# Performance work log

Measured on AMD Instinct MI355X. Metric: run time of the kernel, lower is better.

Reference implementation:

```python
import jax, jax.numpy as jnp
import numpy as np

B, N, M = 16, 4096, 77
Q_DIM, C_DIM = 1024, 768
H, D = 8, 64
INNER = H * D

def setup_inputs() -> dict:
    key = jax.random.key(0)
    ks = jax.random.split(key, 7)
    x = jax.random.normal(ks[0], (B, N, Q_DIM), dtype=jnp.float32)
    context = jax.random.normal(ks[1], (B, M, C_DIM), dtype=jnp.float32)
    # nn.Linear weights (stored as (in, out) for right-multiply), no bias for q/k/v
    Wq = jax.random.normal(ks[2], (Q_DIM, INNER), dtype=jnp.float32) / np.sqrt(Q_DIM)
    Wk = jax.random.normal(ks[3], (C_DIM, INNER), dtype=jnp.float32) / np.sqrt(C_DIM)
    Wv = jax.random.normal(ks[4], (C_DIM, INNER), dtype=jnp.float32) / np.sqrt(C_DIM)
    Wo = jax.random.normal(ks[5], (INNER, Q_DIM), dtype=jnp.float32) / np.sqrt(INNER)
    bo = jax.random.normal(ks[6], (Q_DIM,), dtype=jnp.float32) * 0.01
    return {"x": x, "context": context, "Wq": Wq, "Wk": Wk, "Wv": Wv, "Wo": Wo, "bo": bo}

def reference(x, context, Wq, Wk, Wv, Wo, bo):
    scale = D ** (-0.5)
    q = (x @ Wq).reshape(B, N, H, D).transpose(0, 2, 1, 3)        # (B,H,N,D)
    k = (context @ Wk).reshape(B, M, H, D).transpose(0, 2, 1, 3)  # (B,H,M,D)
    v = (context @ Wv).reshape(B, M, H, D).transpose(0, 2, 1, 3)  # (B,H,M,D)
    attn = jnp.einsum('bhnd,bhmd->bhnm', q, k) * scale            # (B,H,N,M)
    attn = jax.nn.softmax(attn, axis=-1)
    out = jnp.einsum('bhnm,bhmd->bhnd', attn, v)                  # (B,H,N,D)
    out = out.transpose(0, 2, 1, 3).reshape(B, N, INNER)
    return out @ Wo + bo
```

## Files before the change

kernel.cpp:

```cpp
#include <hip/hip_runtime.h>
#include <hip/hip_bf16.h>
#include <stdint.h>


typedef unsigned short u16;
typedef __bf16 bf16x8 __attribute__((ext_vector_type(8)));
typedef float f32x4 __attribute__((ext_vector_type(4)));

__device__ __forceinline__ void gld_lds16(const void* g, void* l) {
  __builtin_amdgcn_global_load_lds(
      (const __attribute__((address_space(1))) unsigned int*)g,
      (__attribute__((address_space(3))) unsigned int*)l, 16, 0, 0);
}

__device__ __forceinline__ u16 f2bf(float f) {
  __hip_bfloat16 h = __float2bfloat16(f);
  return *reinterpret_cast<u16*>(&h);
}

__global__ void wtrans(const float* __restrict__ in, u16* __restrict__ out,
                       int K, int N) {
  int idx = blockIdx.x * 256 + threadIdx.x;
  if (idx < K * N) {
    int n = idx / K, k = idx - n * K;
    out[idx] = f2bf(in[k * N + n]);
  }
}

__global__ void vtrans(const u16* __restrict__ kv_all, u16* __restrict__ vt_all) {
  int idx = blockIdx.x * 256 + threadIdx.x;
  if (idx < 16 * 8 * 64 * 96) {
    int m = idx % 96;
    int t = idx / 96;
    int d = t & 63;
    int bh = t >> 6;
    int b = bh >> 3, h = bh & 7;
    int mg = m < 77 ? m : 76;
    vt_all[idx] = kv_all[(size_t)(b * 77 + mg) * 1024 + 512 + h * 64 + d];
  }
}

template <bool A_F32, bool C_F32>
__global__ __launch_bounds__(256, 2) void gemm_bt(
    const void* __restrict__ Av, const u16* __restrict__ BT,
    void* __restrict__ Cv, const float* __restrict__ bias,
    int Mr, int K, int Nc) {
  __shared__ u16 Al[128 * 32 * (A_F32 ? 2 : 1)];
  __shared__ u16 Bl[128 * 32];
  const int tid = threadIdx.x;
  const int lane = tid & 63;
  const int wave = tid >> 6;
  const int mlane = lane & 15;
  const int quad = lane >> 4;
  const int m0 = blockIdx.y * 128;
  const int n0 = blockIdx.x * 128;
  const int wm = (wave & 1) * 64;
  const int wn = (wave >> 1) * 64;

  f32x4 acc[4][4];
#pragma unroll
  for (int i = 0; i < 4; ++i)
#pragma unroll
    for (int j = 0; j < 4; ++j) acc[i][j] = (f32x4){0.f, 0.f, 0.f, 0.f};

  const int o0 = tid * 16;

  for (int k0 = 0; k0 < K; k0 += 32) {
    if (A_F32) {
#pragma unroll
      for (int r = 0; r < 4; ++r) {
        const int o = r * 4096 + o0;
        const int row = o >> 7;
        const int colb = o & 127;
        int rg = m0 + row;
        rg = rg < Mr ? rg : (Mr - 1);
        gld_lds16((const char*)Av + ((size_t)rg * K + k0) * 4 + colb,
                  (char*)Al + o);
      }
    } else {
#pragma unroll
      for (int r = 0; r < 2; ++r) {
        const int o = r * 4096 + o0;
        const int row = o >> 6;
        const int colb = o & 63;
        int rg = m0 + row;
        rg = rg < Mr ? rg : (Mr - 1);
        gld_lds16((const char*)Av + ((size_t)rg * K + k0) * 2 + colb,
                  (char*)Al + o);
      }
    }
#pragma unroll
    for (int r = 0; r < 2; ++r) {
      const int o = r * 4096 + o0;
      const int row = o >> 6;
      const int colb = o & 63;
      gld_lds16((const char*)BT + ((size_t)(n0 + row) * K + k0) * 2 + colb,
                (char*)Bl + o);
    }
    __syncthreads();

    bf16x8 af[4], bfr[4];
    if (A_F32) {
      const float* Af = (const float*)Al;
#pragma unroll
      for (int i = 0; i < 4; ++i) {
        const float* ar = Af + (wm + i * 16 + mlane) * 32 + quad * 8;
        f32x4 x0 = *(const f32x4*)ar;
        f32x4 x1 = *(const f32x4*)(ar + 4);
        bf16x8 t;
#pragma unroll
        for (int e = 0; e < 4; ++e) {
          u16 lo = f2bf(x0[e]);
          u16 hi = f2bf(x1[e]);
          t[e] = *reinterpret_cast<__bf16*>(&lo);
          t[e + 4] = *reinterpret_cast<__bf16*>(&hi);
        }
        af[i] = t;
      }
    } else {
      const u16* Ab = (const u16*)Al;
#pragma unroll
      for (int i = 0; i < 4; ++i)
        af[i] = *(const bf16x8*)(Ab + (wm + i * 16 + mlane) * 32 + quad * 8);
    }
#pragma unroll
    for (int j = 0; j < 4; ++j)
      bfr[j] = *(const bf16x8*)(Bl + (wn + j * 16 + mlane) * 32 + quad * 8);
#pragma unroll
    for (int i = 0; i < 4; ++i)
#pragma unroll
      for (int j = 0; j < 4; ++j)
        acc[i][j] = __builtin_amdgcn_mfma_f32_16x16x32_bf16(af[i], bfr[j],
                                                            acc[i][j], 0, 0, 0);
    __syncthreads();
  }

#pragma unroll
  for (int j = 0; j < 4; ++j) {
    const int col = n0 + wn + j * 16 + mlane;
    const float bv = C_F32 ? bias[col] : 0.f;
#pragma unroll
    for (int i = 0; i < 4; ++i) {
      const int rb = m0 + wm + i * 16 + quad * 4;
#pragma unroll
      for (int r = 0; r < 4; ++r) {
        const int row = rb + r;
        if (row < Mr) {
          if (C_F32)
            ((float*)Cv)[(size_t)row * Nc + col] = acc[i][j][r] + bv;
          else
            ((u16*)Cv)[(size_t)row * Nc + col] = f2bf(acc[i][j][r]);
        }
      }
    }
  }
}

template <bool A_F32, bool C_F32>
__global__ __launch_bounds__(256, 2) void gemm_bt2(
    const void* __restrict__ Av, const u16* __restrict__ BT,
    void* __restrict__ Cv, const float* __restrict__ bias,
    int Mr, int K, int Nc) {
  __shared__ u16 Al[128 * 32 * (A_F32 ? 2 : 1)];
  __shared__ u16 Bl[256 * 32];
  const int tid = threadIdx.x;
  const int lane = tid & 63;
  const int wave = tid >> 6;
  const int mlane = lane & 15;
  const int quad = lane >> 4;
  const int m0 = blockIdx.y * 128;
  const int n0 = blockIdx.x * 256;
  const int wm = (wave & 1) * 64;
  const int wn = (wave >> 1) * 128;

  f32x4 acc[4][8];
#pragma unroll
  for (int i = 0; i < 4; ++i)
#pragma unroll
    for (int j = 0; j < 8; ++j) acc[i][j] = (f32x4){0.f, 0.f, 0.f, 0.f};

  const int o0 = tid * 16;

  for (int k0 = 0; k0 < K; k0 += 32) {
    if (A_F32) {
#pragma unroll
      for (int r = 0; r < 4; ++r) {
        const int o = r * 4096 + o0;
        const int row = o >> 7;
        const int colb = o & 127;
        int rg = m0 + row;
        rg = rg < Mr ? rg : (Mr - 1);
        gld_lds16((const char*)Av + ((size_t)rg * K + k0) * 4 + colb,
                  (char*)Al + o);
      }
    } else {
#pragma unroll
      for (int r = 0; r < 2; ++r) {
        const int o = r * 4096 + o0;
        const int row = o >> 6;
        const int colb = o & 63;
        int rg = m0 + row;
        rg = rg < Mr ? rg : (Mr - 1);
        gld_lds16((const char*)Av + ((size_t)rg * K + k0) * 2 + colb,
                  (char*)Al + o);
      }
    }
#pragma unroll
    for (int r = 0; r < 4; ++r) {
      const int o = r * 4096 + o0;
      const int row = o >> 6;
      const int colb = o & 63;
      gld_lds16((const char*)BT + ((size_t)(n0 + row) * K + k0) * 2 + colb,
                (char*)Bl + o);
    }
    __syncthreads();

    bf16x8 af[4], bfr[8];
    if (A_F32) {
      const float* Af = (const float*)Al;
#pragma unroll
      for (int i = 0; i < 4; ++i) {
        const float* ar = Af + (wm + i * 16 + mlane) * 32 + quad * 8;
        f32x4 x0 = *(const f32x4*)ar;
        f32x4 x1 = *(const f32x4*)(ar + 4);
        bf16x8 t;
#pragma unroll
        for (int e = 0; e < 4; ++e) {
          u16 lo = f2bf(x0[e]);
          u16 hi = f2bf(x1[e]);
          t[e] = *reinterpret_cast<__bf16*>(&lo);
          t[e + 4] = *reinterpret_cast<__bf16*>(&hi);
        }
        af[i] = t;
      }
    } else {
      const u16* Ab = (const u16*)Al;
#pragma unroll
      for (int i = 0; i < 4; ++i)
        af[i] = *(const bf16x8*)(Ab + (wm + i * 16 + mlane) * 32 + quad * 8);
    }
#pragma unroll
    for (int j = 0; j < 8; ++j)
      bfr[j] = *(const bf16x8*)(Bl + (wn + j * 16 + mlane) * 32 + quad * 8);
#pragma unroll
    for (int i = 0; i < 4; ++i)
#pragma unroll
      for (int j = 0; j < 8; ++j)
        acc[i][j] = __builtin_amdgcn_mfma_f32_16x16x32_bf16(af[i], bfr[j],
                                                            acc[i][j], 0, 0, 0);
    __syncthreads();
  }

#pragma unroll
  for (int j = 0; j < 8; ++j) {
    const int col = n0 + wn + j * 16 + mlane;
    const float bv = C_F32 ? bias[col] : 0.f;
#pragma unroll
    for (int i = 0; i < 4; ++i) {
      const int rb = m0 + wm + i * 16 + quad * 4;
#pragma unroll
      for (int r = 0; r < 4; ++r) {
        const int row = rb + r;
        if (row < Mr) {
          if (C_F32)
            ((float*)Cv)[(size_t)row * Nc + col] = acc[i][j][r] + bv;
          else
            ((u16*)Cv)[(size_t)row * Nc + col] = f2bf(acc[i][j][r]);
        }
      }
    }
  }
}

__global__ __launch_bounds__(256, 2) void attn_mfma(
    const u16* __restrict__ q_all,
    const u16* __restrict__ kv_all,
    const u16* __restrict__ vt_all,
    u16* __restrict__ o_all) {
  __shared__ u16 Ps[128 * 128];
  const int tid = threadIdx.x;
  const int lane = tid & 63;
  const int wave = tid >> 6;
  const int mlane = lane & 15;
  const int quad = lane >> 4;
  const int b = blockIdx.x >> 3;
  const int h = blockIdx.x & 7;
  const int n0 = blockIdx.y * 128;
  const int wm = wave * 32;

  const u16* qbase =
      q_all + ((size_t)(b * 4096 + n0 + wm)) * 512 + h * 64;
  bf16x8 aq[2][2];
#pragma unroll
  for (int i = 0; i < 2; ++i)
#pragma unroll
    for (int ks = 0; ks < 2; ++ks)
      aq[i][ks] = *(const bf16x8*)(qbase + (size_t)(i * 16 + mlane) * 512 +
                                   ks * 32 + quad * 8);

  bf16x8 bk[5][2];
#pragma unroll
  for (int j = 0; j < 5; ++j) {
    int m = j * 16 + mlane;
    m = m < 77 ? m : 76;
    const u16* kb = kv_all + ((size_t)(b * 77 + m)) * 1024 + h * 64;
#pragma unroll
    for (int ks = 0; ks < 2; ++ks)
      bk[j][ks] = *(const bf16x8*)(kb + ks * 32 + quad * 8);
  }

  f32x4 S[2][5];
#pragma unroll
  for (int i = 0; i < 2; ++i)
#pragma unroll
    for (int j = 0; j < 5; ++j) S[i][j] = (f32x4){0.f, 0.f, 0.f, 0.f};
#pragma unroll
  for (int i = 0; i < 2; ++i)
#pragma unroll
    for (int j = 0; j < 5; ++j)
#pragma unroll
      for (int ks = 0; ks < 2; ++ks)
        S[i][j] = __builtin_amdgcn_mfma_f32_16x16x32_bf16(aq[i][ks], bk[j][ks],
                                                          S[i][j], 0, 0, 0);

  float rs[2][4] = {{0.f, 0.f, 0.f, 0.f}, {0.f, 0.f, 0.f, 0.f}};
#pragma unroll
  for (int i = 0; i < 2; ++i)
#pragma unroll
    for (int j = 0; j < 5; ++j) {
      const int col = j * 16 + mlane;
      const bool valid = col < 77;
#pragma unroll
      for (int r = 0; r < 4; ++r) {
        float e = valid ? __expf(S[i][j][r] * 0.125f) : 0.f;
        S[i][j][r] = e;
        rs[i][r] += e;
      }
    }
#pragma unroll
  for (int i = 0; i < 2; ++i)
#pragma unroll
    for (int r = 0; r < 4; ++r) {
      float v = rs[i][r];
      v += __shfl_xor(v, 1);
      v += __shfl_xor(v, 2);
      v += __shfl_xor(v, 4);
      v += __shfl_xor(v, 8);
      rs[i][r] = 1.f / v;
    }

#pragma unroll
  for (int i = 0; i < 2; ++i)
#pragma unroll
    for (int r = 0; r < 4; ++r) {
      const int row = wm + i * 16 + quad * 4 + r;
      u16* prow = Ps + row * 128;
#pragma unroll
      for (int j = 0; j < 5; ++j) {
        const int col = j * 16 + mlane;
        prow[(((col >> 3) + row) & 15) * 8 + (col & 7)] = f2bf(S[i][j][r]);
      }
      const int colz = 80 + mlane;
      prow[(((colz >> 3) + row) & 15) * 8 + (colz & 7)] = 0;
    }
  __syncthreads();

  const u16* vtb = vt_all + (size_t)blockIdx.x * 64 * 96;
  bf16x8 bv[4][3];
#pragma unroll
  for (int j = 0; j < 4; ++j)
#pragma unroll
    for (int kk = 0; kk < 3; ++kk)
      bv[j][kk] = *(const bf16x8*)(vtb + (j * 16 + mlane) * 96 + kk * 32 +
                                   quad * 8);

  f32x4 O[2][4];
#pragma unroll
  for (int i = 0; i < 2; ++i)
#pragma unroll
    for (int j = 0; j < 4; ++j) O[i][j] = (f32x4){0.f, 0.f, 0.f, 0.f};
#pragma unroll
  for (int i = 0; i < 2; ++i) {
    const int row = wm + i * 16 + mlane;
#pragma unroll
    for (int kk = 0; kk < 3; ++kk) {
      const bf16x8 ap = *(const bf16x8*)(
          Ps + row * 128 + (((kk * 4 + quad) + row) & 15) * 8);
#pragma unroll
      for (int j = 0; j < 4; ++j)
        O[i][j] = __builtin_amdgcn_mfma_f32_16x16x32_bf16(ap, bv[j][kk],
                                                          O[i][j], 0, 0, 0);
    }
  }

  u16* ob = o_all + ((size_t)(b * 4096 + n0 + wm)) * 512 + h * 64;
#pragma unroll
  for (int i = 0; i < 2; ++i)
#pragma unroll
    for (int j = 0; j < 4; ++j)
#pragma unroll
      for (int r = 0; r < 4; ++r) {
        const int rl = i * 16 + quad * 4 + r;
        ob[(size_t)rl * 512 + j * 16 + mlane] = f2bf(O[i][j][r] * rs[i][r]);
      }
}

extern "C" void kernel_launch(void* const* d_in, const int* in_sizes, int n_in,
                              void* d_out, int out_size, void* d_ws,
                              size_t ws_size, hipStream_t stream) {
  const float* x = (const float*)d_in[0];
  const float* ctx = (const float*)d_in[1];
  const float* Wq = (const float*)d_in[2];
  const float* Wk = (const float*)d_in[3];
  const float* Wv = (const float*)d_in[4];
  const float* Wo = (const float*)d_in[5];
  const float* bo = (const float*)d_in[6];

  char* p = (char*)d_ws;
  u16* WqT = (u16*)p;  p += (size_t)512 * 1024 * 2;
  u16* WkvT = (u16*)p; p += (size_t)1024 * 768 * 2;
  u16* WoT = (u16*)p;  p += (size_t)1024 * 512 * 2;
  u16* q_all = (u16*)p;    p += (size_t)65536 * 512 * 2;
  u16* kv_all = (u16*)p;   p += (size_t)1232 * 1024 * 2;
  u16* attn_out = (u16*)p; p += (size_t)65536 * 512 * 2;
  u16* vt_all = (u16*)p;   p += (size_t)128 * 64 * 96 * 2;

  wtrans<<<(1024 * 512 + 255) / 256, 256, 0, stream>>>(Wq, WqT, 1024, 512);
  wtrans<<<(768 * 512 + 255) / 256, 256, 0, stream>>>(Wk, WkvT, 768, 512);
  wtrans<<<(768 * 512 + 255) / 256, 256, 0, stream>>>(
      Wv, WkvT + (size_t)512 * 768, 768, 512);
  wtrans<<<(512 * 1024 + 255) / 256, 256, 0, stream>>>(Wo, WoT, 512, 1024);

  gemm_bt2<true, false><<<dim3(2, 512), 256, 0, stream>>>(
      x, WqT, q_all, nullptr, 65536, 1024, 512);
  gemm_bt<true, false><<<dim3(8, 10), 256, 0, stream>>>(
      ctx, WkvT, kv_all, nullptr, 1232, 768, 1024);
  vtrans<<<(128 * 64 * 96 + 255) / 256, 256, 0, stream>>>(kv_all, vt_all);
  attn_mfma<<<dim3(128, 32), 256, 0, stream>>>(q_all, kv_all, vt_all,
                                               attn_out);
  gemm_bt2<false, true><<<dim3(4, 512), 256, 0, stream>>>(
      attn_out, WoT, (void*)d_out, bo, 65536, 512, 1024);
}
```

Before: 737.3 us.

## Replace projection GEMMs with triple-buffered 256x128 tile kernel using swizzled LDS

Both large projection GEMMs (the Q projection and the output projection) now use a new 512-thread kernel with 256x128 output tiles and a 64-wide K step. Tiles are triple-buffered in LDS, so global loads for tile t+2 are issued while MFMAs run on tile t. The fp32 activations are loaded into registers and converted to bf16 before being written to LDS, instead of being converted on every fragment read. The kernel also XOR-swizzles LDS rows to avoid bank conflicts, remaps workgroups for cache locality, and raises wave priority around the MFMA blocks. In exchange it uses about 147KB of LDS, which limits each CU to one workgroup, and it drops the row-bounds checks, so it assumes the dimensions are exact multiples of the tile sizes.

```diff
diff --git a/kernel.cpp b/kernel.cpp
--- a/kernel.cpp
+++ b/kernel.cpp
@@ -156,103 +156,199 @@
   }
 }
 
-template <bool A_F32, bool C_F32>
-__global__ __launch_bounds__(256, 2) void gemm_bt2(
+
+#define DG_STAGE_A_BF16(t_, sl_)                                              \
+  {                                                                           \
+    const char* ab_ =                                                         \
+        (const char*)Av + (size_t)2 * ((size_t)m0 * K + (t_) * 64);           \
+    char* lb_ = lds + (sl_)*DG_BUF;                                           \
+    _Pragma("unroll") for (int c_ = 0; c_ < 4; ++c_) {                        \
+      gld_lds16(ab_ + (size_t)2 * (size_t)(c_ * 64 + arow) * K + asrc,        \
+                lb_ + c_ * 8192 + tid * 16);                                  \
+    }                                                                         \
+  }
+
+#define DG_STAGE_B(t_, sl_)                                                   \
+  {                                                                           \
+    const char* bb_ =                                                         \
+        (const char*)BT + (size_t)2 * ((size_t)n0 * K + (t_) * 64);           \
+    char* lb_ = lds + (sl_)*DG_BUF + 32768;                                   \
+    _Pragma("unroll") for (int c_ = 0; c_ < 2; ++c_) {                        \
+      gld_lds16(bb_ + (size_t)2 * (size_t)(c_ * 64 + arow) * K + asrc,        \
+                lb_ + c_ * 8192 + tid * 16);                                  \
+    }                                                                         \
+  }
+
+#define DG_LOAD_A_F32(t_)                                                     \
+  {                                                                           \
+    const float* af_ = (const float*)Av + (size_t)m0 * K + (t_) * 64;         \
+    _Pragma("unroll") for (int c_ = 0; c_ < 4; ++c_) {                        \
+      const float* s_ = af_ + (size_t)(c_ * 64 + arow) * K + (asrc >> 1);     \
+      sa[2 * c_] = *(const f32x4*)s_;                                         \
+      sa[2 * c_ + 1] = *(const f32x4*)(s_ + 4);                               \
+    }                                                                         \
+  }
+
+#define DG_WRITE_A_F32(sl_)                                                   \
+  {                                                                           \
+    char* lb_ = lds + (sl_)*DG_BUF;                                           \
+    _Pragma("unroll") for (int c_ = 0; c_ < 4; ++c_) {                        \
+      bf16x8 w_;                                                              \
+      _Pragma("unroll") for (int e_ = 0; e_ < 4; ++e_) {                      \
+        u16 lo_ = f2bf(sa[2 * c_][e_]);                                       \
+        u16 hi_ = f2bf(sa[2 * c_ + 1][e_]);                                   \
+        w_[e_] = *reinterpret_cast<__bf16*>(&lo_);                            \
+        w_[e_ + 4] = *reinterpret_cast<__bf16*>(&hi_);                        \
+      }                                                                       \
+      *(bf16x8*)(lb_ + c_ * 8192 + tid * 16) = w_;                            \
+    }                                                                         \
+  }
+
+template <bool A_F32, bool C_F32, int NXL2>
+__global__ __launch_bounds__(512, 2) void gemm_deep(
     const void* __restrict__ Av, const u16* __restrict__ BT,
     void* __restrict__ Cv, const float* __restrict__ bias,
-    int Mr, int K, int Nc) {
-  __shared__ u16 Al[128 * 32 * (A_F32 ? 2 : 1)];
-  __shared__ u16 Bl[256 * 32];
+    const int K, const int Nc) {
+  constexpr int DG_BUF = 49152;
+  __shared__ __align__(16) char lds[3 * DG_BUF];
+
   const int tid = threadIdx.x;
   const int lane = tid & 63;
   const int wave = tid >> 6;
   const int mlane = lane & 15;
   const int quad = lane >> 4;
-  const int m0 = blockIdx.y * 128;
-  const int n0 = blockIdx.x * 256;
-  const int wm = (wave & 1) * 64;
-  const int wn = (wave >> 1) * 128;
-
-  f32x4 acc[4][8];
+  const int wm = (wave >> 1) * 64;
+  const int wn = (wave & 1) * 64;
+  const int rswz = (mlane & 7) << 4;
+
+  const int arow = tid >> 3;
+  const int asrc = ((tid & 7) * 16) ^ ((arow & 7) << 4);
+
+  const int nwg = 256 << NXL2;
+  const int wg = blockIdx.y * (1 << NXL2) + blockIdx.x;
+  const int swz = (wg & 7) * (nwg >> 3) + (wg >> 3);
+  const int m0 = (swz >> NXL2) * 256;
+  const int n0 = (swz & ((1 << NXL2) - 1)) * 128;
+
+  const int nt = K >> 6;
+
+  f32x4 acc[4][4];
 #pragma unroll
   for (int i = 0; i < 4; ++i)
 #pragma unroll
-    for (int j = 0; j < 8; ++j) acc[i][j] = (f32x4){0.f, 0.f, 0.f, 0.f};
-
-  const int o0 = tid * 16;
-
-  for (int k0 = 0; k0 < K; k0 += 32) {
-    if (A_F32) {
-#pragma unroll
-      for (int r = 0; r < 4; ++r) {
-        const int o = r * 4096 + o0;
-        const int row = o >> 7;
-        const int colb = o & 127;
-        int rg = m0 + row;
-        rg = rg < Mr ? rg : (Mr - 1);
-        gld_lds16((const char*)Av + ((size_t)rg * K + k0) * 4 + colb,
-                  (char*)Al + o);
-      }
-    } else {
-#pragma unroll
-      for (int r = 0; r < 2; ++r) {
-        const int o = r * 4096 + o0;
-        const int row = o >> 6;
-        const int colb = o & 63;
-        int rg = m0 + row;
-        rg = rg < Mr ? rg : (Mr - 1);
-        gld_lds16((const char*)Av + ((size_t)rg * K + k0) * 2 + colb,
-                  (char*)Al + o);
-      }
-    }
-#pragma unroll
-    for (int r = 0; r < 4; ++r) {
-      const int o = r * 4096 + o0;
-      const int row = o >> 6;
-      const int colb = o & 63;
-      gld_lds16((const char*)BT + ((size_t)(n0 + row) * K + k0) * 2 + colb,
-                (char*)Bl + o);
-    }
-    __syncthreads();
-
-    bf16x8 af[4], bfr[8];
-    if (A_F32) {
-      const float* Af = (const float*)Al;
-#pragma unroll
-      for (int i = 0; i < 4; ++i) {
-        const float* ar = Af + (wm + i * 16 + mlane) * 32 + quad * 8;
-        f32x4 x0 = *(const f32x4*)ar;
-        f32x4 x1 = *(const f32x4*)(ar + 4);
-        bf16x8 t;
-#pragma unroll
-        for (int e = 0; e < 4; ++e) {
-          u16 lo = f2bf(x0[e]);
-          u16 hi = f2bf(x1[e]);
-          t[e] = *reinterpret_cast<__bf16*>(&lo);
-          t[e + 4] = *reinterpret_cast<__bf16*>(&hi);
+    for (int j = 0; j < 4; ++j) acc[i][j] = (f32x4){0.f, 0.f, 0.f, 0.f};
+
+  f32x4 sa[8];
+
+  if (A_F32) {
+    DG_LOAD_A_F32(0);
+    DG_STAGE_B(0, 0);
+    asm volatile("s_waitcnt vmcnt(2)" ::: "memory");
+    __builtin_amdgcn_sched_barrier(0);
+    DG_WRITE_A_F32(0);
+    DG_LOAD_A_F32(1);
+    DG_STAGE_B(1, 1);
+    asm volatile("s_waitcnt vmcnt(2)" ::: "memory");
+    __builtin_amdgcn_sched_barrier(0);
+    DG_WRITE_A_F32(1);
+    asm volatile("s_waitcnt lgkmcnt(0)" ::: "memory");
+  } else {
+    DG_STAGE_A_BF16(0, 0);
+    DG_STAGE_B(0, 0);
+    DG_STAGE_A_BF16(1, 1);
+    DG_STAGE_B(1, 1);
+    asm volatile("s_waitcnt vmcnt(6)" ::: "memory");
+  }
+  __builtin_amdgcn_sched_barrier(0);
+  __builtin_amdgcn_s_barrier();
+  __builtin_amdgcn_sched_barrier(0);
+
+  int slot = 0;
+  for (int t = 0; t < nt; ++t) {
+    const char* la = lds + slot * DG_BUF;
+    const char* lb = la + 32768;
+    const int t2 = t + 2;
+    const bool do_stage = t2 < nt;
+    const int s2 = (slot >= 1) ? slot - 1 : slot + 2;
+
+    bf16x8 a0[4], b0[4];
+#pragma unroll
+    for (int i = 0; i < 4; ++i)
+      a0[i] = *(const bf16x8*)(la + (wm + i * 16 + mlane) * 128 +
+                               ((quad * 16) ^ rswz));
+#pragma unroll
+    for (int j = 0; j < 4; ++j)
+      b0[j] = *(const bf16x8*)(lb + (wn + j * 16 + mlane) * 128 +
+                               ((quad * 16) ^ rswz));
+    if (do_stage) {
+      if (A_F32) {
+        DG_LOAD_A_F32(t2);
+      } else {
+        DG_STAGE_A_BF16(t2, s2);
+      }
+    }
+    __builtin_amdgcn_sched_barrier(0);
+    __builtin_amdgcn_s_barrier();
+    __builtin_amdgcn_sched_barrier(0);
+    __builtin_amdgcn_s_setprio(1);
+#pragma unroll
+    for (int i = 0; i < 4; ++i)
+#pragma unroll
+      for (int j = 0; j < 4; ++j)
+        acc[i][j] = __builtin_amdgcn_mfma_f32_16x16x32_bf16(a0[i], b0[j],
+                                                            acc[i][j], 0, 0, 0);
+    __builtin_amdgcn_s_setprio(0);
+
+    bf16x8 a1[4], b1[4];
+#pragma unroll
+    for (int i = 0; i < 4; ++i)
+      a1[i] = *(const bf16x8*)(la + (wm + i * 16 + mlane) * 128 +
+                               ((64 + quad * 16) ^ rswz));
+#pragma unroll
+    for (int j = 0; j < 4; ++j)
+      b1[j] = *(const bf16x8*)(lb + (wn + j * 16 + mlane) * 128 +
+                               ((64 + quad * 16) ^ rswz));
+    if (do_stage) {
+      DG_STAGE_B(t2, s2);
+    }
+    __builtin_amdgcn_sched_barrier(0);
+    __builtin_amdgcn_s_barrier();
+    __builtin_amdgcn_sched_barrier(0);
+    __builtin_amdgcn_s_setprio(1);
+#pragma unroll
+    for (int i = 0; i < 4; ++i)
+#pragma unroll
+      for (int j = 0; j < 4; ++j)
+        acc[i][j] = __builtin_amdgcn_mfma_f32_16x16x32_bf16(a1[i], b1[j],
+                                                            acc[i][j], 0, 0, 0);
+    __builtin_amdgcn_s_setprio(0);
+
+    if (t + 1 < nt) {
+      if (A_F32) {
+        if (do_stage) {
+          asm volatile("s_waitcnt vmcnt(2)" ::: "memory");
+          __builtin_amdgcn_sched_barrier(0);
+          DG_WRITE_A_F32(s2);
+          asm volatile("s_waitcnt lgkmcnt(0)" ::: "memory");
+        } else {
+          asm volatile("s_waitcnt vmcnt(0)" ::: "memory");
         }
-        af[i] = t;
-      }
-    } else {
-      const u16* Ab = (const u16*)Al;
-#pragma unroll
-      for (int i = 0; i < 4; ++i)
-        af[i] = *(const bf16x8*)(Ab + (wm + i * 16 + mlane) * 32 + quad * 8);
-    }
-#pragma unroll
-    for (int j = 0; j < 8; ++j)
-      bfr[j] = *(const bf16x8*)(Bl + (wn + j * 16 + mlane) * 32 + quad * 8);
-#pragma unroll
-    for (int i = 0; i < 4; ++i)
-#pragma unroll
-      for (int j = 0; j < 8; ++j)
-        acc[i][j] = __builtin_amdgcn_mfma_f32_16x16x32_bf16(af[i], bfr[j],
-                                                            acc[i][j], 0, 0, 0);
-    __syncthreads();
-  }
-
-#pragma unroll
-  for (int j = 0; j < 8; ++j) {
+      } else {
+        if (do_stage) {
+          asm volatile("s_waitcnt vmcnt(6)" ::: "memory");
+        } else {
+          asm volatile("s_waitcnt vmcnt(0)" ::: "memory");
+        }
+      }
+      __builtin_amdgcn_sched_barrier(0);
+      __builtin_amdgcn_s_barrier();
+      __builtin_amdgcn_sched_barrier(0);
+    }
+    slot = (slot == 2) ? 0 : slot + 1;
+  }
+
+#pragma unroll
+  for (int j = 0; j < 4; ++j) {
     const int col = n0 + wn + j * 16 + mlane;
     const float bv = C_F32 ? bias[col] : 0.f;
 #pragma unroll
@@ -260,13 +356,11 @@
       const int rb = m0 + wm + i * 16 + quad * 4;
 #pragma unroll
       for (int r = 0; r < 4; ++r) {
-        const int row = rb + r;
-        if (row < Mr) {
-          if (C_F32)
-            ((float*)Cv)[(size_t)row * Nc + col] = acc[i][j][r] + bv;
-          else
-            ((u16*)Cv)[(size_t)row * Nc + col] = f2bf(acc[i][j][r]);
-        }
+        const size_t off = (size_t)(rb + r) * Nc + col;
+        if (C_F32)
+          ((float*)Cv)[off] = acc[i][j][r] + bv;
+        else
+          ((u16*)Cv)[off] = f2bf(acc[i][j][r]);
       }
     }
   }
@@ -431,13 +525,13 @@
       Wv, WkvT + (size_t)512 * 768, 768, 512);
   wtrans<<<(512 * 1024 + 255) / 256, 256, 0, stream>>>(Wo, WoT, 512, 1024);
 
-  gemm_bt2<true, false><<<dim3(2, 512), 256, 0, stream>>>(
-      x, WqT, q_all, nullptr, 65536, 1024, 512);
+  gemm_deep<true, false, 2><<<dim3(4, 256), 512, 0, stream>>>(
+      x, WqT, q_all, nullptr, 1024, 512);
   gemm_bt<true, false><<<dim3(8, 10), 256, 0, stream>>>(
       ctx, WkvT, kv_all, nullptr, 1232, 768, 1024);
   vtrans<<<(128 * 64 * 96 + 255) / 256, 256, 0, stream>>>(kv_all, vt_all);
   attn_mfma<<<dim3(128, 32), 256, 0, stream>>>(q_all, kv_all, vt_all,
                                                attn_out);
-  gemm_bt2<false, true><<<dim3(4, 512), 256, 0, stream>>>(
-      attn_out, WoT, (void*)d_out, bo, 65536, 512, 1024);
-}
+  gemm_deep<false, true, 3><<<dim3(8, 256), 512, 0, stream>>>(
+      attn_out, WoT, (void*)d_out, bo, 512, 1024);
+}
```

Result: no change. 723.1 us (-1.9%).

## Replace projection GEMMs with double-buffered 256x256 swizzled-LDS MFMA kernel

Applied to the files above, without the earlier changes.

Adds a separate pass that converts x from fp32 to bf16, writing into the output buffer as scratch. Both large projection GEMMs (Q and output) move to a new 512-thread kernel that uses 256x256 tiles and 64-wide K steps. The new kernel double-buffers LDS with asynchronous global-to-LDS loads, XOR-swizzles LDS to avoid bank conflicts, and interleaves MFMA groups with prefetch using explicit barriers and priority hints. The aim is to remove the fp32 A-load and in-loop conversion overhead and hide memory latency, at the cost of an extra full pass over x and 128KB LDS per block.

```diff
diff --git a/kernel.cpp b/kernel.cpp
--- a/kernel.cpp
+++ b/kernel.cpp
@@ -16,6 +16,23 @@
 __device__ __forceinline__ u16 f2bf(float f) {
   __hip_bfloat16 h = __float2bfloat16(f);
   return *reinterpret_cast<u16*>(&h);
+}
+
+__global__ void cvt8(const float* __restrict__ in, u16* __restrict__ out,
+                     long n8) {
+  long i = (long)blockIdx.x * 256 + threadIdx.x;
+  const long stride = (long)gridDim.x * 256;
+  for (; i < n8; i += stride) {
+    f32x4 x0 = *(const f32x4*)(in + i * 8);
+    f32x4 x1 = *(const f32x4*)(in + i * 8 + 4);
+    union { bf16x8 v; u16 s[8]; } t;
+#pragma unroll
+    for (int e = 0; e < 4; ++e) {
+      t.s[e] = f2bf(x0[e]);
+      t.s[e + 4] = f2bf(x1[e]);
+    }
+    *(bf16x8*)(out + i * 8) = t.v;
+  }
 }
 
 __global__ void wtrans(const float* __restrict__ in, u16* __restrict__ out,
@@ -156,117 +173,145 @@
   }
 }
 
-template <bool A_F32, bool C_F32>
-__global__ __launch_bounds__(256, 2) void gemm_bt2(
-    const void* __restrict__ Av, const u16* __restrict__ BT,
+
+#define ST_A(c_, h_)                                                          \
+  {                                                                           \
+    const char* g_ = (const char*)A +                                         \
+                     (size_t)(m0 + (h_)*128 + srow) * K2 + (size_t)(c_)*128 + \
+                     scol;                                                    \
+    char* d_ = lds + (((c_)&1) * 65536) + (h_)*16384 + sdst;                  \
+    gld_lds16(g_, d_);                                                        \
+    gld_lds16(g_ + (size_t)64 * K2, d_ + 8192);                               \
+  }
+
+#define ST_B(c_, h_)                                                          \
+  {                                                                           \
+    const char* g_ = (const char*)BT +                                        \
+                     (size_t)(n0 + (h_)*128 + srow) * K2 + (size_t)(c_)*128 + \
+                     scol;                                                    \
+    char* d_ = lds + (((c_)&1) * 65536) + 32768 + (h_)*16384 + sdst;          \
+    gld_lds16(g_, d_);                                                        \
+    gld_lds16(g_ + (size_t)64 * K2, d_ + 8192);                               \
+  }
+
+#define LD_A(f_, ks_) \
+  (*(const bf16x8*)(bufc + aoff + (f_)*2048 + (acol ^ ((ks_)*64))))
+#define LD_B(g_, ks_) \
+  (*(const bf16x8*)(bufc + boff + (g_)*2048 + (acol ^ ((ks_)*64))))
+
+#define G8_BAR                                                                \
+  __builtin_amdgcn_sched_barrier(0);                                          \
+  __builtin_amdgcn_s_barrier();                                               \
+  __builtin_amdgcn_sched_barrier(0);
+
+#define G8_MFMA(fb_, ks_)                                                     \
+  G8_BAR;                                                                     \
+  __builtin_amdgcn_s_setprio(1);                                              \
+  _Pragma("unroll") for (int f = 0; f < 4; ++f)                               \
+      _Pragma("unroll") for (int g = 0; g < 4; ++g) acc[(fb_) + f][g] =       \
+          __builtin_amdgcn_mfma_f32_16x16x32_bf16(a[f], b[g][ks_],            \
+                                                  acc[(fb_) + f][g], 0, 0, 0);\
+  __builtin_amdgcn_s_setprio(0);
+
+template <int NX, bool C_F32>
+__global__ __launch_bounds__(512, 2) void gemm8(
+    const u16* __restrict__ A, const u16* __restrict__ BT,
     void* __restrict__ Cv, const float* __restrict__ bias,
-    int Mr, int K, int Nc) {
-  __shared__ u16 Al[128 * 32 * (A_F32 ? 2 : 1)];
-  __shared__ u16 Bl[256 * 32];
+    const int K, const int Nc) {
+  __shared__ __align__(16) char lds[131072];
   const int tid = threadIdx.x;
   const int lane = tid & 63;
   const int wave = tid >> 6;
   const int mlane = lane & 15;
   const int quad = lane >> 4;
-  const int m0 = blockIdx.y * 128;
-  const int n0 = blockIdx.x * 256;
-  const int wm = (wave & 1) * 64;
-  const int wn = (wave >> 1) * 128;
-
-  f32x4 acc[4][8];
-#pragma unroll
-  for (int i = 0; i < 4; ++i)
-#pragma unroll
-    for (int j = 0; j < 8; ++j) acc[i][j] = (f32x4){0.f, 0.f, 0.f, 0.f};
-
-  const int o0 = tid * 16;
-
-  for (int k0 = 0; k0 < K; k0 += 32) {
-    if (A_F32) {
+  const int wmh = wave >> 2;
+  const int wn = (wave & 3) * 64;
+  const size_t K2 = (size_t)K * 2;
+
+  const int nwg = gridDim.x * gridDim.y;
+  const int wg = blockIdx.y * gridDim.x + blockIdx.x;
+  const int swz = (wg & 7) * (nwg >> 3) + (wg >> 3);
+  const int m0 = (swz / NX) * 256;
+  const int n0 = (swz % NX) * 256;
+  const int nkt = K >> 6;
+
+  const int srow = tid >> 3;
+  const int scol = ((tid & 7) * 16) ^ ((srow & 7) << 4);
+  const int sdst = tid * 16;
+
+  const int aoff = wmh * 16384 + mlane * 128;
+  const int boff = 32768 + (wn >> 7) * 16384 + ((wn & 127) + mlane) * 128;
+  const int acol = (quad * 16) ^ ((mlane & 7) << 4);
+
+  f32x4 acc[8][4];
+#pragma unroll
+  for (int i = 0; i < 8; ++i)
+#pragma unroll
+    for (int j = 0; j < 4; ++j) acc[i][j] = (f32x4){0.f, 0.f, 0.f, 0.f};
+
+  ST_B(0, 0);
+  ST_A(0, 0);
+  ST_A(0, 1);
+  ST_B(0, 1);
+  ST_B(1, 0);
+  asm volatile("s_waitcnt vmcnt(2)" ::: "memory");
+  G8_BAR;
+
+  for (int c = 0; c < nkt; ++c) {
+    const char* bufc = lds + ((c & 1) * 65536);
+    const int cp1 = c + 1, cp2 = c + 2;
+    bf16x8 a[4];
+    bf16x8 b[4][2];
+
+#pragma unroll
+    for (int f = 0; f < 4; ++f) a[f] = LD_A(f, 0);
+#pragma unroll
+    for (int g = 0; g < 4; ++g) {
+      b[g][0] = LD_B(g, 0);
+      b[g][1] = LD_B(g, 1);
+    }
+    if (cp1 < nkt) ST_A(cp1, 0);
+    G8_MFMA(0, 0);
+    G8_BAR;
+
+#pragma unroll
+    for (int f = 0; f < 4; ++f) a[f] = LD_A(4 + f, 0);
+    if (cp1 < nkt) ST_A(cp1, 1);
+    G8_MFMA(4, 0);
+    G8_BAR;
+
+#pragma unroll
+    for (int f = 0; f < 4; ++f) a[f] = LD_A(f, 1);
+    if (cp1 < nkt) ST_B(cp1, 1);
+    G8_MFMA(0, 1);
+    G8_BAR;
+
+#pragma unroll
+    for (int f = 0; f < 4; ++f) a[f] = LD_A(4 + f, 1);
+    if (cp2 < nkt) ST_B(cp2, 0);
+    G8_MFMA(4, 1);
+    if (cp2 < nkt) {
+      asm volatile("s_waitcnt vmcnt(2)" ::: "memory");
+    } else {
+      asm volatile("s_waitcnt vmcnt(0)" ::: "memory");
+    }
+    G8_BAR;
+  }
+
+#pragma unroll
+  for (int g = 0; g < 4; ++g) {
+    const int col = n0 + wn + g * 16 + mlane;
+    const float bv = C_F32 ? bias[col] : 0.f;
+#pragma unroll
+    for (int f = 0; f < 8; ++f) {
+      const int row0 = m0 + wmh * 128 + f * 16 + quad * 4;
 #pragma unroll
       for (int r = 0; r < 4; ++r) {
-        const int o = r * 4096 + o0;
-        const int row = o >> 7;
-        const int colb = o & 127;
-        int rg = m0 + row;
-        rg = rg < Mr ? rg : (Mr - 1);
-        gld_lds16((const char*)Av + ((size_t)rg * K + k0) * 4 + colb,
-                  (char*)Al + o);
-      }
-    } else {
-#pragma unroll
-      for (int r = 0; r < 2; ++r) {
-        const int o = r * 4096 + o0;
-        const int row = o >> 6;
-        const int colb = o & 63;
-        int rg = m0 + row;
-        rg = rg < Mr ? rg : (Mr - 1);
-        gld_lds16((const char*)Av + ((size_t)rg * K + k0) * 2 + colb,
-                  (char*)Al + o);
-      }
-    }
-#pragma unroll
-    for (int r = 0; r < 4; ++r) {
-      const int o = r * 4096 + o0;
-      const int row = o >> 6;
-      const int colb = o & 63;
-      gld_lds16((const char*)BT + ((size_t)(n0 + row) * K + k0) * 2 + colb,
-                (char*)Bl + o);
-    }
-    __syncthreads();
-
-    bf16x8 af[4], bfr[8];
-    if (A_F32) {
-      const float* Af = (const float*)Al;
-#pragma unroll
-      for (int i = 0; i < 4; ++i) {
-        const float* ar = Af + (wm + i * 16 + mlane) * 32 + quad * 8;
-        f32x4 x0 = *(const f32x4*)ar;
-        f32x4 x1 = *(const f32x4*)(ar + 4);
-        bf16x8 t;
-#pragma unroll
-        for (int e = 0; e < 4; ++e) {
-          u16 lo = f2bf(x0[e]);
-          u16 hi = f2bf(x1[e]);
-          t[e] = *reinterpret_cast<__bf16*>(&lo);
-          t[e + 4] = *reinterpret_cast<__bf16*>(&hi);
-        }
-        af[i] = t;
-      }
-    } else {
-      const u16* Ab = (const u16*)Al;
-#pragma unroll
-      for (int i = 0; i < 4; ++i)
-        af[i] = *(const bf16x8*)(Ab + (wm + i * 16 + mlane) * 32 + quad * 8);
-    }
-#pragma unroll
-    for (int j = 0; j < 8; ++j)
-      bfr[j] = *(const bf16x8*)(Bl + (wn + j * 16 + mlane) * 32 + quad * 8);
-#pragma unroll
-    for (int i = 0; i < 4; ++i)
-#pragma unroll
-      for (int j = 0; j < 8; ++j)
-        acc[i][j] = __builtin_amdgcn_mfma_f32_16x16x32_bf16(af[i], bfr[j],
-                                                            acc[i][j], 0, 0, 0);
-    __syncthreads();
-  }
-
-#pragma unroll
-  for (int j = 0; j < 8; ++j) {
-    const int col = n0 + wn + j * 16 + mlane;
-    const float bv = C_F32 ? bias[col] : 0.f;
-#pragma unroll
-    for (int i = 0; i < 4; ++i) {
-      const int rb = m0 + wm + i * 16 + quad * 4;
-#pragma unroll
-      for (int r = 0; r < 4; ++r) {
-        const int row = rb + r;
-        if (row < Mr) {
-          if (C_F32)
-            ((float*)Cv)[(size_t)row * Nc + col] = acc[i][j][r] + bv;
-          else
-            ((u16*)Cv)[(size_t)row * Nc + col] = f2bf(acc[i][j][r]);
-        }
+        const size_t off = (size_t)(row0 + r) * Nc + col;
+        if (C_F32)
+          ((float*)Cv)[off] = acc[f][g][r] + bv;
+        else
+          ((u16*)Cv)[off] = f2bf(acc[f][g][r]);
       }
     }
   }
@@ -425,19 +470,23 @@
   u16* attn_out = (u16*)p; p += (size_t)65536 * 512 * 2;
   u16* vt_all = (u16*)p;   p += (size_t)128 * 64 * 96 * 2;
 
+  u16* xb = (u16*)d_out;
+
+  cvt8<<<2048, 256, 0, stream>>>(x, xb, (long)65536 * 1024 / 8);
+
   wtrans<<<(1024 * 512 + 255) / 256, 256, 0, stream>>>(Wq, WqT, 1024, 512);
   wtrans<<<(768 * 512 + 255) / 256, 256, 0, stream>>>(Wk, WkvT, 768, 512);
   wtrans<<<(768 * 512 + 255) / 256, 256, 0, stream>>>(
       Wv, WkvT + (size_t)512 * 768, 768, 512);
   wtrans<<<(512 * 1024 + 255) / 256, 256, 0, stream>>>(Wo, WoT, 512, 1024);
 
-  gemm_bt2<true, false><<<dim3(2, 512), 256, 0, stream>>>(
-      x, WqT, q_all, nullptr, 65536, 1024, 512);
+  gemm8<2, false><<<dim3(2, 256), 512, 0, stream>>>(
+      xb, WqT, q_all, nullptr, 1024, 512);
   gemm_bt<true, false><<<dim3(8, 10), 256, 0, stream>>>(
       ctx, WkvT, kv_all, nullptr, 1232, 768, 1024);
   vtrans<<<(128 * 64 * 96 + 255) / 256, 256, 0, stream>>>(kv_all, vt_all);
   attn_mfma<<<dim3(128, 32), 256, 0, stream>>>(q_all, kv_all, vt_all,
                                                attn_out);
-  gemm_bt2<false, true><<<dim3(4, 512), 256, 0, stream>>>(
-      attn_out, WoT, (void*)d_out, bo, 65536, 512, 1024);
-}
+  gemm8<4, true><<<dim3(4, 256), 512, 0, stream>>>(
+      attn_out, WoT, (void*)d_out, bo, 512, 1024);
+}
```

Result: no change. 726.9 us (-1.4%).
